# Performance work log

Measured on AMD Instinct MI355X. Metric: run time of the kernel, lower is better.

The kernel has to match this reference:

```python
import jax, jax.numpy as jnp
import numpy as np


def setup_inputs() -> dict:
    key = jax.random.key(0)
    k1, k2 = jax.random.split(key)
    x = jax.random.normal(k1, (4, 1, 16384), dtype=jnp.float32)  # [B, C, T]
    # dictionary initialized uniform(-1, 1) as in nn.Parameter(...).uniform_(-1, 1)
    d = jax.random.uniform(k2, (256, 1, 256), dtype=jnp.float32, minval=-1.0, maxval=1.0)  # [A, C, K]
    return {"x": x, "d": d, "n_iterations": 16}


def reference(x, d, n_iterations):
    B, C, T = x.shape
    A, _, K = d.shape
    pad = K // 2
    # normalize each atom over (channels, atom_size) dims, i.e. d_normalization_dims=(-1,-2)
    norms = jnp.linalg.norm(d.reshape(A, -1), axis=-1)
    dn = d / (norms[:, None, None] + 1e-12)

    # work in a padded domain so conv output position == start index in padded residual
    rp = jnp.pad(x, ((0, 0), (0, 0), (pad, pad)))        # residual, [B, C, T+2*pad]
    recon = jnp.zeros_like(rp)                            # accumulated reconstruction
    Tout = T + 2 * pad - K + 1                            # conv output length

    def step(carry, _):
        rp, recon = carry
        # cross-correlation of residual with every atom: [B, A, Tout]
        fm = jax.lax.conv_general_dilated(
            rp, dn, window_strides=(1,), padding='VALID',
            dimension_numbers=('NCH', 'OIH', 'NCH'))
        flat = fm.reshape(B, A * Tout)
        idx = jnp.argmax(flat, axis=-1)                   # signed max, per batch item
        val = jnp.take_along_axis(flat, idx[:, None], axis=-1)[:, 0]
        atom_idx = idx // Tout
        pos = idx % Tout                                  # start index in padded domain
        atoms = dn[atom_idx] * val[:, None, None]         # [B, C, K]

        def upd(r, rec, a, p):
            seg = jax.lax.dynamic_slice(r, (0, p), (C, K))
            r2 = jax.lax.dynamic_update_slice(r, seg - a, (0, p))
            segr = jax.lax.dynamic_slice(rec, (0, p), (C, K))
            rec2 = jax.lax.dynamic_update_slice(rec, segr + a, (0, p))
            return r2, rec2

        rp2, recon2 = jax.vmap(upd)(rp, recon, atoms, pos)
        return (rp2, recon2), None

    (rp, recon), _ = jax.lax.scan(step, (rp, recon), None, length=n_iterations)
    # crop padding -> reconstruction with same shape as x
    return recon[:, :, pad:pad + T]
```

## Files before the change

kernel.cpp:

```cpp
#include <hip/hip_runtime.h>
#include <hip/hip_cooperative_groups.h>
#include <math.h>

namespace cg = cooperative_groups;

#define B    4
#define T    16384
#define A    256
#define K    256
#define PAD  128
#define TP   (T + 2*PAD)
#define TOUT (TP - K + 1)
#define ITERS 16
#define CHUNK 512
#define NCHUNK 33
#define NCP  36
#define TILE 2048
#define NTILE 9
#define NBLK 512

struct Smem {
    float rp[TILE + K + 16];
    float dnA[K];
    float dnB[K];
    float dnsel[K];
    float wv[16]; int wi[16];
    float fv; int fi;
};

#define TAP(acc, s0,s1,s2,s3, dq) { acc = fmaf(s0,(dq).x,acc); acc = fmaf(s1,(dq).y,acc); \
                                    acc = fmaf(s2,(dq).z,acc); acc = fmaf(s3,(dq).w,acc); }

__device__ __forceinline__ void wave_amax(float& bv, int& bi) {
    #pragma unroll
    for (int off = 32; off; off >>= 1) {
        float ov = __shfl_down(bv, off);
        int   oi = __shfl_down(bi, off);
        if (ov > bv || (ov == bv && oi < bi)) { bv = ov; bi = oi; }
    }
}

__device__ __forceinline__ void gbar(unsigned* c, unsigned target) {
    __syncthreads();
    if (threadIdx.x == 0) {
        __hip_atomic_fetch_add(c, 1u, __ATOMIC_RELEASE, __HIP_MEMORY_SCOPE_AGENT);
        while (__hip_atomic_load(c, __ATOMIC_RELAXED, __HIP_MEMORY_SCOPE_AGENT) < target)
            __builtin_amdgcn_s_sleep(2);
        (void)__hip_atomic_load(c, __ATOMIC_ACQUIRE, __HIP_MEMORY_SCOPE_AGENT);
    }
    __syncthreads();
}

__device__ __forceinline__ void dev_norm(int bid, int tid, const float* __restrict__ d,
                                         float* __restrict__ dn, Smem& sm) {
    if (bid < 128) {
        int lane = tid & 63, w = tid >> 6;
        #pragma unroll
        for (int s = 0; s < 2; s++) {
            int atom = (bid & 127)*2 + s;
            float v = d[atom*K + tid];
            float sq = v*v;
            #pragma unroll
            for (int off = 32; off; off >>= 1) sq += __shfl_down(sq, off);
            if (lane == 0) sm.wv[w] = sq;
            __syncthreads();
            float norm = sqrtf(sm.wv[0] + sm.wv[1] + sm.wv[2] + sm.wv[3]) + 1e-12f;
            dn[atom*K + tid] = v / norm;
            __syncthreads();
        }
    }
}

__device__ __forceinline__ void dev_init(int bid, int tid, const float* __restrict__ x,
                                         float* __restrict__ rp, float* __restrict__ recon) {
    for (int i = bid*256 + tid; i < B*TP; i += NBLK*256) {
        int bb = i / TP, t = i - bb*TP;
        float v = (t >= PAD && t < PAD + T) ? x[bb*T + (t - PAD)] : 0.f;
        rp[i] = v;
        recon[i] = 0.f;
    }
}

__device__ void dev_conv(int a0, int b, int tid, const float* __restrict__ rp,
                         const float* __restrict__ dn,
                         float* __restrict__ segval, int* __restrict__ segidx,
                         float* __restrict__ abv, int* __restrict__ abi, Smem& sm) {
    const int aA = a0*2, aB = a0*2 + 1;
    const int lane = tid & 63, w = tid >> 6;
    sm.dnA[tid] = dn[aA*K + tid];
    sm.dnB[tid] = dn[aB*K + tid];
    const float4* rp4 = (const float4*)(rp + (size_t)b*TP);

    for (int tile = 0; tile < NTILE; tile++) {
        int t0 = tile * TILE;
        __syncthreads();
        float4* s4 = (float4*)sm.rp;
        for (int i = tid; i < 580; i += 256) {
            int g = t0/4 + i;
            float4 v = {0.f,0.f,0.f,0.f};
            if (g*4 < TP) v = rp4[g];
            s4[i] = v;
        }
        __syncthreads();
        const float4* srp4 = (const float4*)sm.rp;
        const float4* dA4  = (const float4*)sm.dnA;
        const float4* dB4  = (const float4*)sm.dnB;
        float accA0[4] = {0,0,0,0}, accA1[4] = {0,0,0,0};
        float accB0[4] = {0,0,0,0}, accB1[4] = {0,0,0,0};
        float4 p = srp4[tid];
        float4 q = srp4[tid + 256];
        #pragma unroll 4
        for (int kq = 0; kq < 64; kq++) {
            float4 dA = dA4[kq];
            float4 dB = dB4[kq];
            float4 pn = srp4[tid + kq + 1];
            float4 qn = srp4[tid + 256 + kq + 1];
            TAP(accA0[0], p.x,p.y,p.z,p.w, dA); TAP(accA0[1], p.y,p.z,p.w,pn.x, dA);
            TAP(accA0[2], p.z,p.w,pn.x,pn.y, dA); TAP(accA0[3], p.w,pn.x,pn.y,pn.z, dA);
            TAP(accB0[0], p.x,p.y,p.z,p.w, dB); TAP(accB0[1], p.y,p.z,p.w,pn.x, dB);
            TAP(accB0[2], p.z,p.w,pn.x,pn.y, dB); TAP(accB0[3], p.w,pn.x,pn.y,pn.z, dB);
            TAP(accA1[0], q.x,q.y,q.z,q.w, dA); TAP(accA1[1], q.y,q.z,q.w,qn.x, dA);
            TAP(accA1[2], q.z,q.w,qn.x,qn.y, dA); TAP(accA1[3], q.w,qn.x,qn.y,qn.z, dA);
            TAP(accB1[0], q.x,q.y,q.z,q.w, dB); TAP(accB1[1], q.y,q.z,q.w,qn.x, dB);
            TAP(accB1[2], q.z,q.w,qn.x,qn.y, dB); TAP(accB1[3], q.w,qn.x,qn.y,qn.z, dB);
            p = pn; q = qn;
        }
        int lt = tid * 4;
        float bvA0 = -INFINITY, bvA1 = -INFINITY, bvB0 = -INFINITY, bvB1 = -INFINITY;
        int biA0 = 0x7fffffff, biA1 = 0x7fffffff, biB0 = 0x7fffffff, biB1 = 0x7fffffff;
        #pragma unroll
        for (int j = 0; j < 4; j++) {
            int t = t0 + lt + j;
            if (t < TOUT) {
                if (accA0[j] > bvA0) { bvA0 = accA0[j]; biA0 = aA*TOUT + t; }
                if (accB0[j] > bvB0) { bvB0 = accB0[j]; biB0 = aB*TOUT + t; }
            }
            int t1 = t0 + 1024 + lt + j;
            if (t1 < TOUT) {
                if (accA1[j] > bvA1) { bvA1 = accA1[j]; biA1 = aA*TOUT + t1; }
                if (accB1[j] > bvB1) { bvB1 = accB1[j]; biB1 = aB*TOUT + t1; }
            }
        }
        wave_amax(bvA0, biA0); wave_amax(bvA1, biA1);
        wave_amax(bvB0, biB0); wave_amax(bvB1, biB1);
        if (lane == 0) {
            sm.wv[w]    = bvA0; sm.wi[w]    = biA0;
            sm.wv[4+w]  = bvA1; sm.wi[4+w]  = biA1;
            sm.wv[8+w]  = bvB0; sm.wi[8+w]  = biB0;
            sm.wv[12+w] = bvB1; sm.wi[12+w] = biB1;
        }
        __syncthreads();
        if (tid < 4) {
            float v0 = sm.wv[2*tid];   int i0 = sm.wi[2*tid];
            float v1 = sm.wv[2*tid+1]; int i1 = sm.wi[2*tid+1];
            if (v1 > v0 || (v1 == v0 && i1 < i0)) { v0 = v1; i0 = i1; }
            int chunk = tile*4 + tid;
            if (chunk < NCHUNK) {
                segval[((size_t)b*A + aA)*NCP + chunk] = v0;
                segidx[((size_t)b*A + aA)*NCP + chunk] = i0;
            }
        } else if (tid >= 64 && tid < 68) {
            int c = tid - 64;
            float v0 = sm.wv[8+2*c];   int i0 = sm.wi[8+2*c];
            float v1 = sm.wv[8+2*c+1]; int i1 = sm.wi[8+2*c+1];
            if (v1 > v0 || (v1 == v0 && i1 < i0)) { v0 = v1; i0 = i1; }
            int chunk = tile*4 + c;
            if (chunk < NCHUNK) {
                segval[((size_t)b*A + aB)*NCP + chunk] = v0;
                segidx[((size_t)b*A + aB)*NCP + chunk] = i0;
            }
        }
    }
    __syncthreads();
    if (w < 2) {
        int atom = (w == 0) ? aA : aB;
        float bv = -INFINITY; int bi = 0x7fffffff;
        if (lane < NCHUNK) {
            bv = segval[((size_t)b*A + atom)*NCP + lane];
            bi = segidx[((size_t)b*A + atom)*NCP + lane];
        }
        wave_amax(bv, bi);
        if (lane == 0) { abv[b*A + atom] = bv; abi[b*A + atom] = bi; }
    }
}

__device__ void dev_iter(int a0, int b, int tid, int last,
                         const float* __restrict__ avc, const int* __restrict__ aic,
                         float* __restrict__ avn, int* __restrict__ ain,
                         const float* __restrict__ rin, float* __restrict__ rout,
                         float* __restrict__ recon, const float* __restrict__ dn,
                         float* __restrict__ segval, int* __restrict__ segidx, Smem& sm) {
    const int aA = a0*2, aB = a0*2 + 1;
    const int lane = tid & 63, w = tid >> 6;

    float bv0 = avc[b*A + tid]; int bi0 = aic[b*A + tid];
    const float4* rin4 = (const float4*)(rin + (size_t)b*TP);
    const int icopy = a0*256 + tid;
    const bool docopy = (!last) && (icopy < TP/4);
    float4 vcopy = {0.f,0.f,0.f,0.f};
    if (docopy) vcopy = rin4[icopy];
    sm.dnA[tid] = dn[aA*K + tid];
    sm.dnB[tid] = dn[aB*K + tid];

    {
        float bv = bv0; int bi = bi0;
        wave_amax(bv, bi);
        if (lane == 0) { sm.wv[w] = bv; sm.wi[w] = bi; }
        __syncthreads();
        if (tid == 0) {
            bv = sm.wv[0]; bi = sm.wi[0];
            for (int j = 1; j < 4; j++)
                if (sm.wv[j] > bv || (sm.wv[j] == bv && sm.wi[j] < bi)) { bv = sm.wv[j]; bi = sm.wi[j]; }
            sm.fv = bv; sm.fi = bi;
        }
        __syncthreads();
    }
    float val = sm.fv; int idx = sm.fi;
    int atom = idx / TOUT, pos = idx - atom*TOUT;
    sm.dnsel[tid] = dn[atom*K + tid];

    int lo = pos - (K-1); if (lo < 0) lo = 0;
    int c_lo = lo >> 9;
    int tbase = c_lo * CHUNK;

    if (!last) {
        float4* s4 = (float4*)sm.rp;
        for (int i = tid; i < 324; i += 256) {
            int g = tbase/4 + i;
            float4 v = {0.f,0.f,0.f,0.f};
            if (g*4 < TP) v = rin4[g];
            s4[i] = v;
        }
    }
    __syncthreads();
    if (docopy) {
        float4* rout4 = (float4*)(rout + (size_t)b*TP);
        float4 v = vcopy;
        int o = icopy*4 - pos;
        if (o > -4 && o < K) {
            if (o+0 >= 0 && o+0 < K) v.x -= val * sm.dnsel[o+0];
            if (o+1 >= 0 && o+1 < K) v.y -= val * sm.dnsel[o+1];
            if (o+2 >= 0 && o+2 < K) v.z -= val * sm.dnsel[o+2];
            if (o+3 >= 0 && o+3 < K) v.w -= val * sm.dnsel[o+3];
        }
        rout4[icopy] = v;
    }
    if (a0 == 0) {
        recon[(size_t)b*TP + pos + tid] += val * sm.dnsel[tid];
    }
    if (last) return;

    sm.rp[pos + tid - tbase] -= val * sm.dnsel[tid];
    __syncthreads();

    const float4* srp4 = (const float4*)sm.rp;
    const float4* dA4  = (const float4*)sm.dnA;
    const float4* dB4  = (const float4*)sm.dnB;
    float cA[4] = {0,0,0,0}, cB[4] = {0,0,0,0};
    float4 p = srp4[tid];
    #pragma unroll 4
    for (int kq = 0; kq < 64; kq++) {
        float4 dA = dA4[kq];
        float4 dB = dB4[kq];
        float4 pn = srp4[tid + kq + 1];
        TAP(cA[0], p.x,p.y,p.z,p.w, dA); TAP(cA[1], p.y,p.z,p.w,pn.x, dA);
        TAP(cA[2], p.z,p.w,pn.x,pn.y, dA); TAP(cA[3], p.w,pn.x,pn.y,pn.z, dA);
        TAP(cB[0], p.x,p.y,p.z,p.w, dB); TAP(cB[1], p.y,p.z,p.w,pn.x, dB);
        TAP(cB[2], p.z,p.w,pn.x,pn.y, dB); TAP(cB[3], p.w,pn.x,pn.y,pn.z, dB);
        p = pn;
    }
    int lt = tid * 4;
    float bvA = -INFINITY, bvB = -INFINITY;
    int biA = 0x7fffffff, biB = 0x7fffffff;
    #pragma unroll
    for (int j = 0; j < 4; j++) {
        int t = tbase + lt + j;
        if (t < TOUT) {
            if (cA[j] > bvA) { bvA = cA[j]; biA = aA*TOUT + t; }
            if (cB[j] > bvB) { bvB = cB[j]; biB = aB*TOUT + t; }
        }
    }
    wave_amax(bvA, biA); wave_amax(bvB, biB);
    if (lane == 0) { sm.wv[w] = bvA; sm.wi[w] = biA; sm.wv[8+w] = bvB; sm.wi[8+w] = biB; }
    __syncthreads();
    if (tid < 2) {
        float v0 = sm.wv[2*tid];   int i0 = sm.wi[2*tid];
        float v1 = sm.wv[2*tid+1]; int i1 = sm.wi[2*tid+1];
        if (v1 > v0 || (v1 == v0 && i1 < i0)) { v0 = v1; i0 = i1; }
        int chunk = c_lo + tid;
        if (chunk < NCHUNK) {
            segval[((size_t)b*A + aA)*NCP + chunk] = v0;
            segidx[((size_t)b*A + aA)*NCP + chunk] = i0;
        }
    } else if (tid >= 64 && tid < 66) {
        int c = tid - 64;
        float v0 = sm.wv[8+2*c];   int i0 = sm.wi[8+2*c];
        float v1 = sm.wv[8+2*c+1]; int i1 = sm.wi[8+2*c+1];
        if (v1 > v0 || (v1 == v0 && i1 < i0)) { v0 = v1; i0 = i1; }
        int chunk = c_lo + c;
        if (chunk < NCHUNK) {
            segval[((size_t)b*A + aB)*NCP + chunk] = v0;
            segidx[((size_t)b*A + aB)*NCP + chunk] = i0;
        }
    }
    __syncthreads();
    if (w < 2) {
        int at = (w == 0) ? aA : aB;
        float bv = -INFINITY; int bi = 0x7fffffff;
        if (lane < NCHUNK) {
            bv = segval[((size_t)b*A + at)*NCP + lane];
            bi = segidx[((size_t)b*A + at)*NCP + lane];
        }
        wave_amax(bv, bi);
        if (lane == 0) { avn[b*A + at] = bv; ain[b*A + at] = bi; }
    }
}

__global__ void __launch_bounds__(256, 2)
k_coop(const float* __restrict__ x, const float* __restrict__ d, float* __restrict__ out,
       float* __restrict__ dn, float* __restrict__ rp0, float* __restrict__ rp1,
       float* __restrict__ recon, float* __restrict__ segval, int* __restrict__ segidx,
       float* __restrict__ abv0, int* __restrict__ abi0,
       float* __restrict__ abv1, int* __restrict__ abi1, unsigned* __restrict__ bar) {
    __shared__ Smem sm;
    const int bid = blockIdx.x, tid = threadIdx.x;
    const int a0 = bid & 127, b = bid >> 7;
    unsigned gen = 0;
    dev_norm(bid, tid, d, dn, sm);
    dev_init(bid, tid, x, rp0, recon);
    gen++; gbar(bar, gen*NBLK);
    dev_conv(a0, b, tid, rp0, dn, segval, segidx, abv0, abi0, sm);
    gen++; gbar(bar, gen*NBLK);
    const float* rin = rp0; float* rout = rp1;
    const float* avc = abv0; const int* aic = abi0;
    float* avn = abv1; int* ain = abi1;
    for (int it = 0; it < ITERS-1; it++) {
        dev_iter(a0, b, tid, 0, avc, aic, avn, ain,
                 rin, rout, recon, dn, segval, segidx, sm);
        { const float* t1 = rin; rin = rout; rout = (float*)t1; }
        { const float* t2 = avc; avc = avn; avn = (float*)t2; }
        { const int*   t3 = aic; aic = ain; ain = (int*)t3; }
        gen++; gbar(bar, gen*NBLK);
    }
    if (a0 == 0) {
        dev_iter(a0, b, tid, 1, avc, aic, avn, ain,
                 rin, rout, recon, dn, segval, segidx, sm);
        const float4* rc4 = (const float4*)(recon + (size_t)b*TP + PAD);
        float4* o4 = (float4*)(out + (size_t)b*T);
        for (int i = tid; i < T/4; i += 256) o4[i] = rc4[i];
    }
}

__global__ void __launch_bounds__(256) k_f_norm_init(const float* x, const float* d,
                                                     float* dn, float* rp0, float* recon) {
    __shared__ Smem sm;
    dev_norm(blockIdx.x, threadIdx.x, d, dn, sm);
    dev_init(blockIdx.x, threadIdx.x, x, rp0, recon);
}
__global__ void __launch_bounds__(256, 2) k_f_conv(const float* rp, const float* dn,
                                                   float* segval, int* segidx,
                                                   float* abv, int* abi) {
    __shared__ Smem sm;
    dev_conv(blockIdx.x & 127, blockIdx.x >> 7, threadIdx.x, rp, dn, segval, segidx, abv, abi, sm);
}
__global__ void __launch_bounds__(256, 2) k_f_iter(int last,
                                                   const float* avc, const int* aic,
                                                   float* avn, int* ain,
                                                   const float* rin, float* rout,
                                                   float* recon, const float* dn,
                                                   float* segval, int* segidx) {
    __shared__ Smem sm;
    dev_iter(blockIdx.x & 127, blockIdx.x >> 7, threadIdx.x, last,
             avc, aic, avn, ain, rin, rout, recon, dn, segval, segidx, sm);
}
__global__ void k_f_out(const float* recon, float* out) {
    int i = blockIdx.x * blockDim.x + threadIdx.x;
    if (i >= B*T) return;
    int b = i / T, t = i - b*T;
    out[i] = recon[(size_t)b*TP + PAD + t];
}

extern "C" void kernel_launch(void* const* d_in, const int* in_sizes, int n_in,
                              void* d_out, int out_size, void* d_ws, size_t ws_size,
                              hipStream_t stream) {
    const float* x = (const float*)d_in[0];
    const float* d = (const float*)d_in[1];
    float* out = (float*)d_out;

    float* ws     = (float*)d_ws;
    float* dn     = ws;
    float* rp0    = dn  + (size_t)A*K;
    float* rp1    = rp0 + (size_t)B*TP;
    float* recon  = rp1 + (size_t)B*TP;
    float* segval = recon + (size_t)B*TP;
    int*   segidx = (int*)(segval + (size_t)B*A*NCP);
    float* abv0   = (float*)(segidx + (size_t)B*A*NCP);
    float* abv1   = abv0 + (size_t)B*A;
    int*   abi0   = (int*)(abv1 + (size_t)B*A);
    int*   abi1   = abi0 + (size_t)B*A;
    unsigned* bar = (unsigned*)(abi1 + (size_t)B*A);

    int nb = 0, ncu = 0;
    hipError_t e1 = hipOccupancyMaxActiveBlocksPerMultiprocessor(&nb, (const void*)k_coop, 256, 0);
    hipError_t e2 = hipDeviceGetAttribute(&ncu, hipDeviceAttributeMultiprocessorCount, 0);
    bool coop = (e1 == hipSuccess && e2 == hipSuccess && nb > 0 && ncu > 0 &&
                 (long)nb * ncu >= NBLK);
    if (coop) {
        (void)hipMemsetAsync(bar, 0, 64, stream);
        void* args[] = {(void*)&x, (void*)&d, (void*)&out, (void*)&dn,
                        (void*)&rp0, (void*)&rp1, (void*)&recon,
                        (void*)&segval, (void*)&segidx,
                        (void*)&abv0, (void*)&abi0, (void*)&abv1, (void*)&abi1,
                        (void*)&bar};
        hipError_t e = hipLaunchCooperativeKernel((const void*)k_coop, dim3(NBLK), dim3(256),
                                                  args, 0, stream);
        if (e == hipSuccess) return;
    }
    k_f_norm_init<<<NBLK, 256, 0, stream>>>(x, d, dn, rp0, recon);
    k_f_conv<<<NBLK, 256, 0, stream>>>(rp0, dn, segval, segidx, abv0, abi0);
    float* rbuf[2] = {rp0, rp1};
    float* av[2]   = {abv0, abv1};
    int*   ai[2]   = {abi0, abi1};
    for (int it = 0; it < ITERS; it++) {
        k_f_iter<<<NBLK, 256, 0, stream>>>(it == ITERS-1 ? 1 : 0,
                                           av[it & 1], ai[it & 1],
                                           av[(it + 1) & 1], ai[(it + 1) & 1],
                                           rbuf[it & 1], rbuf[(it + 1) & 1],
                                           recon, dn, segval, segidx);
    }
    k_f_out<<<(B*T + 255)/256, 256, 0, stream>>>(recon, out);
}
```

Before: 544.7 us.

## Replace grid-wide barrier with independent per-batch barriers on separate cache lines

Each batch item's group of 128 blocks now synchronises only among itself, using a counter padded onto its own cache line, instead of all 512 blocks spinning on one global counter. To make the groups independent, every group normalises the full dictionary redundantly and initialises only its own batch row of the residual and reconstruction. This is meant to cut barrier latency and atomic contention and to let batches drift out of lockstep. In exchange it adds redundant normalisation work and racing identical writes to the shared normalised dictionary, and it zeroes a larger barrier region.

```diff
diff --git a/kernel.cpp b/kernel.cpp
--- a/kernel.cpp
+++ b/kernel.cpp
@@ -18,6 +18,8 @@
 #define TILE 2048
 #define NTILE 9
 #define NBLK 512
+#define BPB  128
+#define BARSTRIDE 64
 
 struct Smem {
     float rp[TILE + K + 16];
@@ -51,33 +53,31 @@
     __syncthreads();
 }
 
-__device__ __forceinline__ void dev_norm(int bid, int tid, const float* __restrict__ d,
+__device__ __forceinline__ void dev_norm(int a0, int tid, const float* __restrict__ d,
                                          float* __restrict__ dn, Smem& sm) {
-    if (bid < 128) {
-        int lane = tid & 63, w = tid >> 6;
+    int lane = tid & 63, w = tid >> 6;
+    #pragma unroll
+    for (int s = 0; s < 2; s++) {
+        int atom = a0*2 + s;
+        float v = d[atom*K + tid];
+        float sq = v*v;
         #pragma unroll
-        for (int s = 0; s < 2; s++) {
-            int atom = (bid & 127)*2 + s;
-            float v = d[atom*K + tid];
-            float sq = v*v;
-            #pragma unroll
-            for (int off = 32; off; off >>= 1) sq += __shfl_down(sq, off);
-            if (lane == 0) sm.wv[w] = sq;
-            __syncthreads();
-            float norm = sqrtf(sm.wv[0] + sm.wv[1] + sm.wv[2] + sm.wv[3]) + 1e-12f;
-            dn[atom*K + tid] = v / norm;
-            __syncthreads();
-        }
-    }
-}
-
-__device__ __forceinline__ void dev_init(int bid, int tid, const float* __restrict__ x,
+        for (int off = 32; off; off >>= 1) sq += __shfl_down(sq, off);
+        if (lane == 0) sm.wv[w] = sq;
+        __syncthreads();
+        float norm = sqrtf(sm.wv[0] + sm.wv[1] + sm.wv[2] + sm.wv[3]) + 1e-12f;
+        dn[atom*K + tid] = v / norm;
+        __syncthreads();
+    }
+}
+
+__device__ __forceinline__ void dev_init(int a0, int b, int tid, const float* __restrict__ x,
                                          float* __restrict__ rp, float* __restrict__ recon) {
-    for (int i = bid*256 + tid; i < B*TP; i += NBLK*256) {
-        int bb = i / TP, t = i - bb*TP;
-        float v = (t >= PAD && t < PAD + T) ? x[bb*T + (t - PAD)] : 0.f;
-        rp[i] = v;
-        recon[i] = 0.f;
+    int i = a0*256 + tid;
+    if (i < TP) {
+        float v = (i >= PAD && i < PAD + T) ? x[b*T + (i - PAD)] : 0.f;
+        rp[(size_t)b*TP + i] = v;
+        recon[(size_t)b*TP + i] = 0.f;
     }
 }
 
@@ -325,12 +325,13 @@
     __shared__ Smem sm;
     const int bid = blockIdx.x, tid = threadIdx.x;
     const int a0 = bid & 127, b = bid >> 7;
+    unsigned* cb = bar + b*BARSTRIDE;
     unsigned gen = 0;
-    dev_norm(bid, tid, d, dn, sm);
-    dev_init(bid, tid, x, rp0, recon);
-    gen++; gbar(bar, gen*NBLK);
+    dev_norm(a0, tid, d, dn, sm);
+    dev_init(a0, b, tid, x, rp0, recon);
+    gen++; gbar(cb, gen*BPB);
     dev_conv(a0, b, tid, rp0, dn, segval, segidx, abv0, abi0, sm);
-    gen++; gbar(bar, gen*NBLK);
+    gen++; gbar(cb, gen*BPB);
     const float* rin = rp0; float* rout = rp1;
     const float* avc = abv0; const int* aic = abi0;
     float* avn = abv1; int* ain = abi1;
@@ -340,7 +341,7 @@
         { const float* t1 = rin; rin = rout; rout = (float*)t1; }
         { const float* t2 = avc; avc = avn; avn = (float*)t2; }
         { const int*   t3 = aic; aic = ain; ain = (int*)t3; }
-        gen++; gbar(bar, gen*NBLK);
+        gen++; gbar(cb, gen*BPB);
     }
     if (a0 == 0) {
         dev_iter(a0, b, tid, 1, avc, aic, avn, ain,
@@ -354,8 +355,8 @@
 __global__ void __launch_bounds__(256) k_f_norm_init(const float* x, const float* d,
                                                      float* dn, float* rp0, float* recon) {
     __shared__ Smem sm;
-    dev_norm(blockIdx.x, threadIdx.x, d, dn, sm);
-    dev_init(blockIdx.x, threadIdx.x, x, rp0, recon);
+    dev_norm(blockIdx.x & 127, threadIdx.x, d, dn, sm);
+    dev_init(blockIdx.x & 127, blockIdx.x >> 7, threadIdx.x, x, rp0, recon);
 }
 __global__ void __launch_bounds__(256, 2) k_f_conv(const float* rp, const float* dn,
                                                    float* segval, int* segidx,
@@ -406,7 +407,7 @@
     bool coop = (e1 == hipSuccess && e2 == hipSuccess && nb > 0 && ncu > 0 &&
                  (long)nb * ncu >= NBLK);
     if (coop) {
-        (void)hipMemsetAsync(bar, 0, 64, stream);
+        (void)hipMemsetAsync(bar, 0, B*BARSTRIDE*sizeof(unsigned), stream);
         void* args[] = {(void*)&x, (void*)&d, (void*)&out, (void*)&dn,
                         (void*)&rp0, (void*)&rp1, (void*)&recon,
                         (void*)&segval, (void*)&segidx,
```

New measurement: 545.8 us. No clear change (+0.2%).
